# Kernel optimization log

Hardware: AMD Instinct MI355X
Metric: run time of the kernel (lower is better)

Reference implementation:

```python
import jax, jax.numpy as jnp
import numpy as np
import math

V, D, L, M, S, B = 32000, 1024, 4, 4096, 2048, 4


def sinusoidal_positional_encoding(max_seq_len, embedding_dim):
    position = jnp.arange(max_seq_len, dtype=jnp.float32)[:, None]
    div_term = jnp.exp(jnp.arange(0, embedding_dim, 2, dtype=jnp.float32)
                       * (-math.log(10000.0) / embedding_dim))
    pe = jnp.zeros((max_seq_len, embedding_dim), jnp.float32)
    pe = pe.at[:, 0::2].set(jnp.sin(position * div_term))
    pe = pe.at[:, 1::2].set(jnp.cos(position * div_term))
    return pe


def setup_inputs() -> dict:
    key = jax.random.key(0)
    ks = jax.random.split(key, 12)
    s = 0.02
    return {
        "x": jax.random.randint(ks[0], (B, S), 0, V, dtype=jnp.int64),
        "emb": jax.random.normal(ks[1], (V, D), jnp.float32) * s,
        "pos_enc": sinusoidal_positional_encoding(S, D),
        "wq": jax.random.normal(ks[2], (D, D), jnp.float32) * s,
        "bq": jnp.zeros((D,), jnp.float32),
        "wk": jax.random.normal(ks[3], (D, D), jnp.float32) * s,
        "bk": jnp.zeros((D,), jnp.float32),
        "wv": jax.random.normal(ks[4], (D, D), jnp.float32) * s,
        "bv": jnp.zeros((D,), jnp.float32),
        "w1s": jax.random.normal(ks[5], (L, D, M), jnp.float32) * s,
        "b1s": jnp.zeros((L, M), jnp.float32),
        "w2s": jax.random.normal(ks[6], (L, M, D), jnp.float32) * s,
        "b2s": jnp.zeros((L, D), jnp.float32),
    }


def reference(x, emb, pos_enc, wq, bq, wk, bk, wv, bv, w1s, b1s, w2s, b2s):
    seq = x.shape[1]
    h = emb[x] + pos_enc[:seq]                      # [B,S,D]
    q = h @ wq + bq
    k = h @ wk + bk
    v = h @ wv + bv
    scores = jnp.einsum('bqd,bkd->bqk', q, k) / jnp.sqrt(jnp.float32(k.shape[-1]))
    # Faithful to source: triu(diagonal=0) KEPT -> attends to self and future.
    mask = jnp.triu(jnp.ones((seq, seq), bool), k=0)
    scores = jnp.where(mask, scores, -jnp.inf)
    attn = jax.nn.softmax(scores, axis=-1)
    h = jax.nn.relu(jnp.einsum('bqk,bkd->bqd', attn, v))
    for i in range(w1s.shape[0]):
        h = jax.nn.relu(h @ w1s[i] + b1s[i])
        h = jax.nn.relu(h @ w2s[i] + b2s[i])
    return h
```

## Files before the change

kernel.cpp:

```cpp
#include <hip/hip_runtime.h>

#define D_DIM 1024
#define S_DIM 2048
#define B_DIM 4
#define M_DIM 4096
#define NTOK  8192

typedef unsigned short u16;
typedef __attribute__((ext_vector_type(8))) short short8;
typedef __attribute__((ext_vector_type(4))) float fx4;

static __device__ __forceinline__ float b2f(u16 u) {
  union { unsigned int i; float f; } v; v.i = ((unsigned int)u) << 16; return v.f;
}
static __device__ __forceinline__ u16 f2b(float f) {
  union { float f; unsigned int i; } v; v.f = f;
  unsigned int r = v.i + 0x7fffu + ((v.i >> 16) & 1u);
  return (u16)(r >> 16);
}
static __device__ __forceinline__ void async16(u16* lds, const u16* g) {
  __builtin_amdgcn_global_load_lds(
      (__attribute__((address_space(1))) void*)(u16*)g,
      (__attribute__((address_space(3))) void*)lds, 16, 0, 0);
}

__global__ void canary_kernel(float* __restrict__ out) {
  const long i = ((long)blockIdx.x * 256 + threadIdx.x) * 4;
  float4 v = {1.0f, 1.0f, 1.0f, 1.0f};
  *(float4*)(out + i) = v;
}

__global__ void Transformer_33792802685820_kernel(
    const int* __restrict__ x, const float* __restrict__ emb,
    const float* __restrict__ pe, u16* __restrict__ h) {
  const int t = blockIdx.x;
  const int s = t & (S_DIM - 1);
  const int row = x[t];
  const int d = threadIdx.x * 4;
  float4 e = *(const float4*)(emb + (long)row * D_DIM + d);
  float4 p = *(const float4*)(pe + (long)s * D_DIM + d);
  ushort4 o;
  o.x = f2b(e.x + p.x);
  o.y = f2b(e.y + p.y);
  o.z = f2b(e.z + p.z);
  o.w = f2b(e.w + p.w);
  *(ushort4*)(h + (long)t * D_DIM + d) = o;
}

__global__ void transpose_f_kernel(
    const float* __restrict__ in, u16* __restrict__ out, int R, int C) {
  __shared__ float tile[32][33];
  const int c0 = blockIdx.x * 32, r0 = blockIdx.y * 32;
  const int tx = threadIdx.x, ty = threadIdx.y;
  for (int i = ty; i < 32; i += 8)
    tile[i][tx] = in[(long)(r0 + i) * C + (c0 + tx)];
  __syncthreads();
  for (int i = ty; i < 32; i += 8)
    out[(long)(c0 + i) * R + (r0 + tx)] = f2b(tile[tx][i]);
}

__global__ void transpose_b_kernel(
    const u16* __restrict__ in, u16* __restrict__ out, int R, int C) {
  __shared__ u16 tile[32][33];
  const long zoff = (long)blockIdx.z * R * C;
  const int c0 = blockIdx.x * 32, r0 = blockIdx.y * 32;
  const int tx = threadIdx.x, ty = threadIdx.y;
  for (int i = ty; i < 32; i += 8)
    tile[i][tx] = in[zoff + (long)(r0 + i) * C + (c0 + tx)];
  __syncthreads();
  for (int i = ty; i < 32; i += 8)
    out[zoff + (long)(c0 + i) * R + (r0 + tx)] = tile[tx][i];
}

template<bool RELU, bool BIAS, bool OUTF32>
__global__ __launch_bounds__(512) void gemm8p(
    const u16* __restrict__ A, const u16* __restrict__ Bt,
    const float* __restrict__ bias, u16* __restrict__ C, float* __restrict__ Cf,
    int M, int N, int K, float scale, long sA_, long sB_, long sC_) {
  __shared__ u16 sA0[16384];
  __shared__ u16 sA1[16384];
  __shared__ u16 sB0[16384];
  __shared__ u16 sB1[16384];

  const int tid  = threadIdx.x;
  const int lane = tid & 63;
  const int wave = tid >> 6;
  const int quad = lane >> 4;
  const int l16  = lane & 15;
  const int wm   = wave >> 2;
  const int wn   = wave & 3;

  const int gx  = gridDim.x;
  const int nwg = gx * gridDim.y;
  const int id0 = blockIdx.y * gx + blockIdx.x;
  const int cpx = nwg >> 3;
  const int sid = (id0 & 7) * cpx + (id0 >> 3);
  const int n0  = (sid % gx) << 8;
  const int m0  = (sid / gx) << 8;

  A  += (long)blockIdx.z * sA_;
  Bt += (long)blockIdx.z * sB_;

  const int srow = tid >> 2;
  const int pc   = tid & 3;
  const int lc   = pc ^ (srow & 3);
  const u16* gA0 = A  + (long)(m0 + srow) * K + lc * 8;
  const u16* gB0 = Bt + (long)(n0 + srow) * K + lc * 8;
  const int ldst = tid << 3;

  const int cko = ((quad ^ (l16 & 3)) << 3);
  const int baA = wm * 4096 + l16 * 32 + cko;
  const int baB = (wn >> 1) * 4096 + (((wn & 1) << 6) + l16) * 32 + cko;

  fx4 acc[8][4] = {};
  short8 ar[4], br[4];

  const int NT = K >> 6;

#define STG_A(S, t, kk) do { \
    const long ko_ = (long)(t) * 64 + (kk) * 32; \
    async16(&S[(kk) * 8192 + ldst],        gA0 + ko_); \
    async16(&S[(kk) * 8192 + 4096 + ldst], gA0 + (long)128 * K + ko_); \
  } while (0)
#define STG_B(S, t, kk) do { \
    const long ko_ = (long)(t) * 64 + (kk) * 32; \
    async16(&S[(kk) * 8192 + ldst],        gB0 + ko_); \
    async16(&S[(kk) * 8192 + 4096 + ldst], gB0 + (long)128 * K + ko_); \
  } while (0)
#define RD_A(S, mh, kk) do { \
    _Pragma("unroll") for (int i_ = 0; i_ < 4; ++i_) \
      ar[i_] = *(const short8*)&S[(kk) * 8192 + baA + ((mh) * 64 + i_ * 16) * 32]; \
  } while (0)
#define RD_B(S, kk) do { \
    _Pragma("unroll") for (int n_ = 0; n_ < 4; ++n_) \
      br[n_] = *(const short8*)&S[(kk) * 8192 + baB + n_ * 512]; \
  } while (0)
#define MM(mh) do { \
    __builtin_amdgcn_s_setprio(1); \
    _Pragma("unroll") for (int i_ = 0; i_ < 4; ++i_) \
      _Pragma("unroll") for (int n_ = 0; n_ < 4; ++n_) \
        acc[(mh) * 4 + i_][n_] = __builtin_amdgcn_mfma_f32_16x16x32_bf16( \
            ar[i_], br[n_], acc[(mh) * 4 + i_][n_], 0, 0, 0); \
    __builtin_amdgcn_s_setprio(0); \
  } while (0)
#define BARR  __builtin_amdgcn_s_barrier()
#define LGKM  asm volatile("s_waitcnt lgkmcnt(0)")
#define VM6   asm volatile("s_waitcnt vmcnt(6)")
#define VM0   asm volatile("s_waitcnt vmcnt(0)")

  STG_B(sB0, 0, 0); STG_A(sA0, 0, 0); STG_B(sB0, 0, 1); STG_A(sA0, 0, 1);
  STG_B(sB1, 1, 0); STG_A(sA1, 1, 0); STG_B(sB1, 1, 1);
  VM6; BARR;

  for (int t = 0; t < NT; t += 2) {
    const bool more = (t + 2 < NT);
    RD_A(sA0, 0, 0); RD_B(sB0, 0);
    STG_A(sA1, t + 1, 1);
    BARR; LGKM; MM(0);
    RD_A(sA0, 1, 0);
    if (more) STG_B(sB0, t + 2, 0);
    BARR; LGKM; MM(1);
    RD_A(sA0, 0, 1); RD_B(sB0, 1);
    if (more) STG_A(sA0, t + 2, 0);
    BARR; LGKM; MM(0);
    RD_A(sA0, 1, 1);
    if (more) { STG_B(sB0, t + 2, 1); VM6; } else { VM0; }
    BARR; LGKM; MM(1);
    RD_A(sA1, 0, 0); RD_B(sB1, 0);
    if (more) STG_A(sA0, t + 2, 1);
    BARR; LGKM; MM(0);
    RD_A(sA1, 1, 0);
    if (more) STG_B(sB1, t + 3, 0);
    BARR; LGKM; MM(1);
    RD_A(sA1, 0, 1); RD_B(sB1, 1);
    if (more) STG_A(sA1, t + 3, 0);
    BARR; LGKM; MM(0);
    RD_A(sA1, 1, 1);
    if (more) { STG_B(sB1, t + 3, 1); VM6; }
    BARR; LGKM; MM(1);
  }

  float bv[4];
  #pragma unroll
  for (int n = 0; n < 4; ++n)
    bv[n] = BIAS ? bias[n0 + wn * 64 + n * 16 + l16] : 0.0f;

  #pragma unroll
  for (int f = 0; f < 8; ++f) {
    #pragma unroll
    for (int r = 0; r < 4; ++r) {
      const long row  = m0 + wm * 128 + f * 16 + quad * 4 + r;
      const long base = (long)blockIdx.z * sC_ + row * N + n0 + wn * 64 + l16;
      #pragma unroll
      for (int n = 0; n < 4; ++n) {
        float v = acc[f][n][r] * scale + bv[n];
        if (RELU) { if (v < 0.0f) v = 0.0f; }
        if (OUTF32) Cf[base + n * 16] = v;
        else        C [base + n * 16] = f2b(v);
      }
    }
  }
#undef STG_A
#undef STG_B
#undef RD_A
#undef RD_B
#undef MM
#undef BARR
#undef LGKM
#undef VM6
#undef VM0
}

__global__ void softmax_kernel(u16* __restrict__ P) {
  const int q = blockIdx.x;
  u16* p = P + ((long)blockIdx.y * S_DIM + q) * S_DIM;
  const int tid = threadIdx.x;
  const int wave = tid >> 6, lane = tid & 63;
  __shared__ float red[4];
  float vals[8];
  float mx = -3.0e38f;
  for (int it = 0; it < 8; ++it) {
    int k = tid + it * 256;
    float v = (k >= q) ? b2f(p[k]) : -3.0e38f;
    vals[it] = v;
    mx = fmaxf(mx, v);
  }
  for (int off = 32; off > 0; off >>= 1)
    mx = fmaxf(mx, __shfl_down(mx, off, 64));
  if (lane == 0) red[wave] = mx;
  __syncthreads();
  mx = fmaxf(fmaxf(red[0], red[1]), fmaxf(red[2], red[3]));
  __syncthreads();
  float sum = 0.0f;
  for (int it = 0; it < 8; ++it) {
    int k = tid + it * 256;
    float e = (k >= q) ? __expf(vals[it] - mx) : 0.0f;
    vals[it] = e;
    sum += e;
  }
  for (int off = 32; off > 0; off >>= 1)
    sum += __shfl_down(sum, off, 64);
  if (lane == 0) red[wave] = sum;
  __syncthreads();
  sum = red[0] + red[1] + red[2] + red[3];
  const float inv = 1.0f / sum;
  for (int it = 0; it < 8; ++it) {
    int k = tid + it * 256;
    p[k] = f2b(vals[it] * inv);
  }
}

extern "C" void kernel_launch(void* const* d_in, const int* in_sizes, int n_in,
                              void* d_out, int out_size, void* d_ws, size_t ws_size,
                              hipStream_t stream) {
  (void)in_sizes; (void)n_in; (void)out_size; (void)ws_size;
  const int*   x   = (const int*)d_in[0];
  const float* emb = (const float*)d_in[1];
  const float* pe  = (const float*)d_in[2];
  const float* wq  = (const float*)d_in[3];
  const float* bq  = (const float*)d_in[4];
  const float* wk  = (const float*)d_in[5];
  const float* bk  = (const float*)d_in[6];
  const float* wv  = (const float*)d_in[7];
  const float* bv  = (const float*)d_in[8];
  const float* w1s = (const float*)d_in[9];
  const float* b1s = (const float*)d_in[10];
  const float* w2s = (const float*)d_in[11];
  const float* b2s = (const float*)d_in[12];
  float* out = (float*)d_out;

  u16* ws  = (u16*)d_ws;
  u16* h   = ws;
  u16* q   = h  + (long)NTOK * D_DIM;
  u16* kx  = q  + (long)NTOK * D_DIM;
  u16* v   = kx + (long)NTOK * D_DIM;
  u16* P   = v  + (long)NTOK * D_DIM;
  u16* wqT = P  + (long)B_DIM * S_DIM * S_DIM;
  u16* wkT = wqT + (long)D_DIM * D_DIM;
  u16* wvT = wkT + (long)D_DIM * D_DIM;
  u16* w1T = wvT + (long)D_DIM * D_DIM;
  u16* w2T = w1T + (long)D_DIM * M_DIM;
  u16* vT  = q;
  u16* mb  = kx;

  const dim3 blk256(256);
  const dim3 blk512(512);
  const dim3 blkT(32, 8);

  canary_kernel<<<dim3(NTOK), blk256, 0, stream>>>(out);

  transpose_f_kernel<<<dim3(32, 32), blkT, 0, stream>>>(wq, wqT, 1024, 1024);
  transpose_f_kernel<<<dim3(32, 32), blkT, 0, stream>>>(wk, wkT, 1024, 1024);
  transpose_f_kernel<<<dim3(32, 32), blkT, 0, stream>>>(wv, wvT, 1024, 1024);

  Transformer_33792802685820_kernel<<<dim3(NTOK), blk256, 0, stream>>>(x, emb, pe, h);

  gemm8p<false, true, false><<<dim3(4, 32, 1), blk512, 0, stream>>>(h, wqT, bq, q,  nullptr, NTOK, D_DIM, D_DIM, 1.0f, 0, 0, 0);
  gemm8p<false, true, false><<<dim3(4, 32, 1), blk512, 0, stream>>>(h, wkT, bk, kx, nullptr, NTOK, D_DIM, D_DIM, 1.0f, 0, 0, 0);
  gemm8p<false, true, false><<<dim3(4, 32, 1), blk512, 0, stream>>>(h, wvT, bv, v,  nullptr, NTOK, D_DIM, D_DIM, 1.0f, 0, 0, 0);

  gemm8p<false, false, false><<<dim3(8, 8, 4), blk512, 0, stream>>>(q, kx, nullptr, P, nullptr,
      S_DIM, S_DIM, D_DIM, 0.03125f, (long)S_DIM * D_DIM, (long)S_DIM * D_DIM, (long)S_DIM * S_DIM);

  softmax_kernel<<<dim3(S_DIM, B_DIM), blk256, 0, stream>>>(P);

  transpose_b_kernel<<<dim3(32, 64, 4), blkT, 0, stream>>>(v, vT, 2048, 1024);
  gemm8p<true, false, false><<<dim3(4, 8, 4), blk512, 0, stream>>>(P, vT, nullptr, h, nullptr,
      S_DIM, D_DIM, S_DIM, 1.0f, (long)S_DIM * S_DIM, (long)D_DIM * S_DIM, (long)S_DIM * D_DIM);

  for (int i = 0; i < 4; ++i) {
    transpose_f_kernel<<<dim3(128, 32), blkT, 0, stream>>>(w1s + (long)i * D_DIM * M_DIM, w1T, 1024, 4096);
    transpose_f_kernel<<<dim3(32, 128), blkT, 0, stream>>>(w2s + (long)i * D_DIM * M_DIM, w2T, 4096, 1024);
    gemm8p<true, true, false><<<dim3(16, 32, 1), blk512, 0, stream>>>(
        h, w1T, b1s + i * M_DIM, mb, nullptr, NTOK, M_DIM, D_DIM, 1.0f, 0, 0, 0);
    if (i == 3)
      gemm8p<true, true, true><<<dim3(4, 32, 1), blk512, 0, stream>>>(
          mb, w2T, b2s + i * D_DIM, nullptr, out, NTOK, D_DIM, M_DIM, 1.0f, 0, 0, 0);
    else
      gemm8p<true, true, false><<<dim3(4, 32, 1), blk512, 0, stream>>>(
          mb, w2T, b2s + i * D_DIM, h, nullptr, NTOK, D_DIM, M_DIM, 1.0f, 0, 0, 0);
  }
}
```

Baseline: 1.192 ms.

## Add narrower-tile GEMM variants for QKV and N=1024 GEMMs; skip masked softmax work

Adds a simple 128x128 gemm_bt kernel that replaces the 256x256 pipelined kernel for the three QKV projections. It also adds gemm8n, a 256x128-tile variant of the pipelined kernel, used for P·V and the second FFN GEMM so the N=1024 GEMMs launch twice as many workgroups and fill more CUs. Softmax now skips loading and exponentiating 256-wide chunks that lie entirely before the diagonal and writes zeros there directly. The simpler QKV kernel has no double buffering and syncs twice per k-step, which may lower its per-CU throughput.

```diff
diff --git a/kernel.cpp b/kernel.cpp
--- a/kernel.cpp
+++ b/kernel.cpp
@@ -73,6 +73,84 @@
 }
 
 template<bool RELU, bool BIAS, bool OUTF32>
+__global__ void gemm_bt(
+    const u16* __restrict__ A, const u16* __restrict__ Bt,
+    const float* __restrict__ bias, u16* __restrict__ C, float* __restrict__ Cf,
+    int M, int N, int K, float scale, long sA, long sB, long sC) {
+  __shared__ u16 As[128 * 32];
+  __shared__ u16 Bs[128 * 32];
+  const int tid  = threadIdx.x;
+  const int wave = tid >> 6;
+  const int lane = tid & 63;
+  const int quad = lane >> 4;
+  const int l16  = lane & 15;
+  const int wm = (wave & 1) << 6;
+  const int wn = (wave >> 1) << 6;
+  A  += (long)blockIdx.z * sA;
+  Bt += (long)blockIdx.z * sB;
+  const int m0 = blockIdx.y << 7;
+  const int n0 = blockIdx.x << 7;
+
+  const int row_a = tid >> 2;
+  const int c4    = (tid & 3) << 3;
+  const u16* gA = A  + (long)(m0 + row_a) * K + c4;
+  const u16* gB = Bt + (long)(n0 + row_a) * K + c4;
+  u16* lA = &As[tid * 8];
+  u16* lB = &Bs[tid * 8];
+
+  fx4 acc[4][4] = {};
+
+  for (int k0 = 0; k0 < K; k0 += 32) {
+    async16(lA,            gA + k0);
+    async16(lA + 64 * 32,  gA + (long)64 * K + k0);
+    async16(lB,            gB + k0);
+    async16(lB + 64 * 32,  gB + (long)64 * K + k0);
+    __syncthreads();
+    short8 af[4], bfv[4];
+    #pragma unroll
+    for (int i = 0; i < 4; ++i) {
+      af[i]  = *(const short8*)&As[(wm + i * 16 + l16) * 32 + quad * 8];
+      bfv[i] = *(const short8*)&Bs[(wn + i * 16 + l16) * 32 + quad * 8];
+    }
+    __syncthreads();
+    #pragma unroll
+    for (int mi = 0; mi < 4; ++mi)
+      #pragma unroll
+      for (int ni = 0; ni < 4; ++ni)
+        acc[mi][ni] = __builtin_amdgcn_mfma_f32_16x16x32_bf16(
+            af[mi], bfv[ni], acc[mi][ni], 0, 0, 0);
+  }
+
+  float bv[4];
+  #pragma unroll
+  for (int ni = 0; ni < 4; ++ni)
+    bv[ni] = BIAS ? bias[n0 + wn + ni * 16 + l16] : 0.0f;
+
+  #pragma unroll
+  for (int mi = 0; mi < 4; ++mi) {
+    #pragma unroll
+    for (int r = 0; r < 4; ++r) {
+      const long row = m0 + wm + mi * 16 + quad * 4 + r;
+      const long base = row * N + n0 + wn + l16;
+      #pragma unroll
+      for (int ni = 0; ni < 4; ++ni) {
+        float v = acc[mi][ni][r] * scale + bv[ni];
+        if (RELU) { if (v < 0.0f) v = 0.0f; }
+        if (OUTF32) Cf[(long)blockIdx.z * sC + base + ni * 16] = v;
+        else        C [(long)blockIdx.z * sC + base + ni * 16] = f2b(v);
+      }
+    }
+  }
+}
+
+#define BARR  __builtin_amdgcn_s_barrier()
+#define LGKM  asm volatile("s_waitcnt lgkmcnt(0)")
+#define VM8   asm volatile("s_waitcnt vmcnt(8)")
+#define VM6   asm volatile("s_waitcnt vmcnt(6)")
+#define VM3   asm volatile("s_waitcnt vmcnt(3)")
+#define VM0   asm volatile("s_waitcnt vmcnt(0)")
+
+template<bool RELU, bool BIAS, bool OUTF32>
 __global__ __launch_bounds__(512) void gemm8p(
     const u16* __restrict__ A, const u16* __restrict__ Bt,
     const float* __restrict__ bias, u16* __restrict__ C, float* __restrict__ Cf,
@@ -143,10 +221,6 @@
             ar[i_], br[n_], acc[(mh) * 4 + i_][n_], 0, 0, 0); \
     __builtin_amdgcn_s_setprio(0); \
   } while (0)
-#define BARR  __builtin_amdgcn_s_barrier()
-#define LGKM  asm volatile("s_waitcnt lgkmcnt(0)")
-#define VM6   asm volatile("s_waitcnt vmcnt(6)")
-#define VM0   asm volatile("s_waitcnt vmcnt(0)")
 
   STG_B(sB0, 0, 0); STG_A(sA0, 0, 0); STG_B(sB0, 0, 1); STG_A(sA0, 0, 1);
   STG_B(sB1, 1, 0); STG_A(sA1, 1, 0); STG_B(sB1, 1, 1);
@@ -205,10 +279,134 @@
 #undef RD_A
 #undef RD_B
 #undef MM
-#undef BARR
-#undef LGKM
-#undef VM6
-#undef VM0
+}
+
+template<bool RELU, bool BIAS, bool OUTF32>
+__global__ __launch_bounds__(512) void gemm8n(
+    const u16* __restrict__ A, const u16* __restrict__ Bt,
+    const float* __restrict__ bias, u16* __restrict__ C, float* __restrict__ Cf,
+    int M, int N, int K, float scale, long sA_, long sB_, long sC_) {
+  __shared__ u16 sA0[16384];
+  __shared__ u16 sA1[16384];
+  __shared__ u16 sB0[8192];
+  __shared__ u16 sB1[8192];
+
+  const int tid  = threadIdx.x;
+  const int lane = tid & 63;
+  const int wave = tid >> 6;
+  const int quad = lane >> 4;
+  const int l16  = lane & 15;
+  const int wm   = wave >> 1;
+  const int wn   = wave & 1;
+
+  const int gx  = gridDim.x;
+  const int nwg = gx * gridDim.y;
+  const int id0 = blockIdx.y * gx + blockIdx.x;
+  const int cpx = nwg >> 3;
+  const int sid = (id0 & 7) * cpx + (id0 >> 3);
+  const int n0  = (sid % gx) << 7;
+  const int m0  = (sid / gx) << 8;
+
+  A  += (long)blockIdx.z * sA_;
+  Bt += (long)blockIdx.z * sB_;
+
+  const int srow = tid >> 2;
+  const int pc   = tid & 3;
+  const int lc   = pc ^ (srow & 3);
+  const u16* gA0 = A  + (long)(m0 + srow) * K + lc * 8;
+  const u16* gB0 = Bt + (long)(n0 + srow) * K + lc * 8;
+  const int ldst = tid << 3;
+
+  const int cko = ((quad ^ (l16 & 3)) << 3);
+  const int baA = (wm >> 1) * 4096 + (((wm & 1) << 6) + l16) * 32 + cko;
+  const int baB = ((wn << 6) + l16) * 32 + cko;
+
+  fx4 acc[4][4] = {};
+  short8 ar[4], br[2];
+
+  const int NT = K >> 6;
+
+#define STG_A(S, t, kk) do { \
+    const long ko_ = (long)(t) * 64 + (kk) * 32; \
+    async16(&S[(kk) * 8192 + ldst],        gA0 + ko_); \
+    async16(&S[(kk) * 8192 + 4096 + ldst], gA0 + (long)128 * K + ko_); \
+  } while (0)
+#define STG_B(S, t, kk) \
+    async16(&S[(kk) * 4096 + ldst], gB0 + (long)(t) * 64 + (kk) * 32)
+#define RD_A(S, kk) do { \
+    _Pragma("unroll") for (int i_ = 0; i_ < 4; ++i_) \
+      ar[i_] = *(const short8*)&S[(kk) * 8192 + baA + i_ * 512]; \
+  } while (0)
+#define RD_B(S, kk, nh) do { \
+    _Pragma("unroll") for (int n_ = 0; n_ < 2; ++n_) \
+      br[n_] = *(const short8*)&S[(kk) * 4096 + baB + ((nh) * 2 + n_) * 512]; \
+  } while (0)
+#define MM(nh) do { \
+    __builtin_amdgcn_s_setprio(1); \
+    _Pragma("unroll") for (int i_ = 0; i_ < 4; ++i_) \
+      _Pragma("unroll") for (int n_ = 0; n_ < 2; ++n_) \
+        acc[i_][(nh) * 2 + n_] = __builtin_amdgcn_mfma_f32_16x16x32_bf16( \
+            ar[i_], br[n_], acc[i_][(nh) * 2 + n_], 0, 0, 0); \
+    __builtin_amdgcn_s_setprio(0); \
+  } while (0)
+
+  STG_A(sA0, 0, 0); STG_B(sB0, 0, 0); STG_A(sA0, 0, 1); STG_B(sB0, 0, 1);
+  STG_A(sA1, 1, 0); STG_B(sB1, 1, 0); STG_A(sA1, 1, 1);
+  VM8; BARR;
+
+  for (int t = 0; t < NT; t += 2) {
+    const bool more = (t + 2 < NT);
+    RD_A(sA0, 0); RD_B(sB0, 0, 0);
+    STG_B(sB1, t + 1, 1);
+    BARR; LGKM; MM(0);
+    RD_B(sB0, 0, 1);
+    if (more) { STG_A(sA0, t + 2, 0); VM8; } else { VM6; }
+    BARR; LGKM; MM(1);
+    RD_A(sA0, 1); RD_B(sB0, 1, 0);
+    if (more) STG_B(sB0, t + 2, 0);
+    BARR; LGKM; MM(0);
+    RD_B(sB0, 1, 1);
+    if (more) { STG_A(sA0, t + 2, 1); VM8; } else { VM3; }
+    BARR; LGKM; MM(1);
+    RD_A(sA1, 0); RD_B(sB1, 0, 0);
+    if (more) STG_B(sB0, t + 2, 1);
+    BARR; LGKM; MM(0);
+    RD_B(sB1, 0, 1);
+    if (more) { STG_A(sA1, t + 3, 0); VM8; } else { VM0; }
+    BARR; LGKM; MM(1);
+    RD_A(sA1, 1); RD_B(sB1, 1, 0);
+    if (more) STG_B(sB1, t + 3, 0);
+    BARR; LGKM; MM(0);
+    RD_B(sB1, 1, 1);
+    if (more) { STG_A(sA1, t + 3, 1); VM8; }
+    BARR; LGKM; MM(1);
+  }
+
+  float bv[4];
+  #pragma unroll
+  for (int n = 0; n < 4; ++n)
+    bv[n] = BIAS ? bias[n0 + wn * 64 + n * 16 + l16] : 0.0f;
+
+  #pragma unroll
+  for (int f = 0; f < 4; ++f) {
+    #pragma unroll
+    for (int r = 0; r < 4; ++r) {
+      const long row  = m0 + wm * 64 + f * 16 + quad * 4 + r;
+      const long base = (long)blockIdx.z * sC_ + row * N + n0 + wn * 64 + l16;
+      #pragma unroll
+      for (int n = 0; n < 4; ++n) {
+        float v = acc[f][n][r] * scale + bv[n];
+        if (RELU) { if (v < 0.0f) v = 0.0f; }
+        if (OUTF32) Cf[base + n * 16] = v;
+        else        C [base + n * 16] = f2b(v);
+      }
+    }
+  }
+#undef STG_A
+#undef STG_B
+#undef RD_A
+#undef RD_B
+#undef MM
 }
 
 __global__ void softmax_kernel(u16* __restrict__ P) {
@@ -216,10 +414,12 @@
   u16* p = P + ((long)blockIdx.y * S_DIM + q) * S_DIM;
   const int tid = threadIdx.x;
   const int wave = tid >> 6, lane = tid & 63;
+  const int it0 = q >> 8;
   __shared__ float red[4];
   float vals[8];
+  for (int it = 0; it < it0; ++it) p[tid + it * 256] = 0;
   float mx = -3.0e38f;
-  for (int it = 0; it < 8; ++it) {
+  for (int it = it0; it < 8; ++it) {
     int k = tid + it * 256;
     float v = (k >= q) ? b2f(p[k]) : -3.0e38f;
     vals[it] = v;
@@ -232,7 +432,7 @@
   mx = fmaxf(fmaxf(red[0], red[1]), fmaxf(red[2], red[3]));
   __syncthreads();
   float sum = 0.0f;
-  for (int it = 0; it < 8; ++it) {
+  for (int it = it0; it < 8; ++it) {
     int k = tid + it * 256;
     float e = (k >= q) ? __expf(vals[it] - mx) : 0.0f;
     vals[it] = e;
@@ -244,7 +444,7 @@
   __syncthreads();
   sum = red[0] + red[1] + red[2] + red[3];
   const float inv = 1.0f / sum;
-  for (int it = 0; it < 8; ++it) {
+  for (int it = it0; it < 8; ++it) {
     int k = tid + it * 256;
     p[k] = f2b(vals[it] * inv);
   }
@@ -295,9 +495,9 @@
 
   Transformer_33792802685820_kernel<<<dim3(NTOK), blk256, 0, stream>>>(x, emb, pe, h);
 
-  gemm8p<false, true, false><<<dim3(4, 32, 1), blk512, 0, stream>>>(h, wqT, bq, q,  nullptr, NTOK, D_DIM, D_DIM, 1.0f, 0, 0, 0);
-  gemm8p<false, true, false><<<dim3(4, 32, 1), blk512, 0, stream>>>(h, wkT, bk, kx, nullptr, NTOK, D_DIM, D_DIM, 1.0f, 0, 0, 0);
-  gemm8p<false, true, false><<<dim3(4, 32, 1), blk512, 0, stream>>>(h, wvT, bv, v,  nullptr, NTOK, D_DIM, D_DIM, 1.0f, 0, 0, 0);
+  gemm_bt<false, true, false><<<dim3(8, 64, 1), blk256, 0, stream>>>(h, wqT, bq, q,  nullptr, NTOK, D_DIM, D_DIM, 1.0f, 0, 0, 0);
+  gemm_bt<false, true, false><<<dim3(8, 64, 1), blk256, 0, stream>>>(h, wkT, bk, kx, nullptr, NTOK, D_DIM, D_DIM, 1.0f, 0, 0, 0);
+  gemm_bt<false, true, false><<<dim3(8, 64, 1), blk256, 0, stream>>>(h, wvT, bv, v,  nullptr, NTOK, D_DIM, D_DIM, 1.0f, 0, 0, 0);
 
   gemm8p<false, false, false><<<dim3(8, 8, 4), blk512, 0, stream>>>(q, kx, nullptr, P, nullptr,
       S_DIM, S_DIM, D_DIM, 0.03125f, (long)S_DIM * D_DIM, (long)S_DIM * D_DIM, (long)S_DIM * S_DIM);
@@ -305,7 +505,7 @@
   softmax_kernel<<<dim3(S_DIM, B_DIM), blk256, 0, stream>>>(P);
 
   transpose_b_kernel<<<dim3(32, 64, 4), blkT, 0, stream>>>(v, vT, 2048, 1024);
-  gemm8p<true, false, false><<<dim3(4, 8, 4), blk512, 0, stream>>>(P, vT, nullptr, h, nullptr,
+  gemm8n<true, false, false><<<dim3(8, 8, 4), blk512, 0, stream>>>(P, vT, nullptr, h, nullptr,
       S_DIM, D_DIM, S_DIM, 1.0f, (long)S_DIM * S_DIM, (long)D_DIM * S_DIM, (long)S_DIM * D_DIM);
 
   for (int i = 0; i < 4; ++i) {
@@ -314,10 +514,10 @@
     gemm8p<true, true, false><<<dim3(16, 32, 1), blk512, 0, stream>>>(
         h, w1T, b1s + i * M_DIM, mb, nullptr, NTOK, M_DIM, D_DIM, 1.0f, 0, 0, 0);
     if (i == 3)
-      gemm8p<true, true, true><<<dim3(4, 32, 1), blk512, 0, stream>>>(
+      gemm8n<true, true, true><<<dim3(8, 32, 1), blk512, 0, stream>>>(
           mb, w2T, b2s + i * D_DIM, nullptr, out, NTOK, D_DIM, M_DIM, 1.0f, 0, 0, 0);
     else
-      gemm8p<true, true, false><<<dim3(4, 32, 1), blk512, 0, stream>>>(
+      gemm8n<true, true, false><<<dim3(8, 32, 1), blk512, 0, stream>>>(
           mb, w2T, b2s + i * D_DIM, h, nullptr, NTOK, D_DIM, M_DIM, 1.0f, 0, 0, 0);
   }
 }
```

New measurement: 1.159 ms. -2.8%, faster.
